# Kernel optimization log

Hardware: AMD Instinct MI355X
Metric: run time of the kernel (lower is better)

Reference implementation:

```python
import jax, jax.numpy as jnp
import numpy as np

C, K, H = 256, 64, 1024


def squash(t):
    # t: [C, H]; norm = sum of squares over last dim (matches torch code)
    norm = jnp.sum(t * t, axis=-1, keepdims=True)  # [C, 1]
    scale = norm / (1.0 + norm)
    return scale * t / jnp.sqrt(norm)


def setup_inputs() -> dict:
    key = jax.random.key(0)
    k1, k2 = jax.random.split(key)
    encoder_output = jax.random.normal(k1, (C, K, H), dtype=jnp.float32)
    # nn.Linear weight [out, in]; scaled init for numerical sanity
    W = jax.random.normal(k2, (H, H), dtype=jnp.float32) * (1.0 / np.sqrt(H))
    return {"encoder_output": encoder_output, "W": W, "iter_routing": 3}


def reference(encoder_output, W, iter_routing):
    # encoder_output: [C, K, H], W: [H, H] (l_1 weight, no bias)
    # The linear projection is loop-invariant in the original; hoist it.
    x_hat = jnp.einsum('ckh,dh->ckd', encoder_output, W)  # [C, K, H]
    b = jnp.zeros(encoder_output.shape[:2], dtype=encoder_output.dtype)  # [C, K]
    c = None
    for _ in range(iter_routing):
        d = jax.nn.softmax(b, axis=-1)                       # [C, K]
        c_hat = jnp.sum(x_hat * d[..., None], axis=1)        # [C, H]
        c = squash(c_hat)                                    # [C, H]
        b = b + jnp.einsum('ckh,ch->ck', x_hat, c)           # [C, K]
    return c
```

## Files before the change

### kernel.cpp

```cpp
#include <hip/hip_runtime.h>


using f32x4  = __attribute__((ext_vector_type(4))) float;
using f32x2  = __attribute__((ext_vector_type(2))) float;
using bf16x8 = __attribute__((ext_vector_type(8))) __bf16;
using bf16x2 = __attribute__((ext_vector_type(2))) __bf16;

struct BfPair { __bf16 hi, lo; };
__device__ inline BfPair split_bf16(float x) {
    BfPair p;
    p.hi = (__bf16)x;
    p.lo = (__bf16)(x - (float)p.hi);
    return p;
}

template <int MODE>
__global__ __launch_bounds__(1024) void routing_kernel(
    const float* __restrict__ enc, const float* __restrict__ u0,
    const float* __restrict__ u1, float* __restrict__ bglob,
    __bf16* __restrict__ s_hi, __bf16* __restrict__ s_lo)
{
    __shared__ float spart[16][1024];
    __shared__ float b_s[64];
    __shared__ float d_s[64];

    const int t = threadIdx.x, lane = t & 63, w = t >> 6;
    const int c = blockIdx.x;
    const float* E = enc + (size_t)c * 65536;

    f32x4 er[4][4];
    #pragma unroll
    for (int r = 0; r < 4; ++r) {
        const float* ek = E + (size_t)(w * 4 + r) * 1024 + lane * 8;
        er[r][0] = *(const f32x4*)(ek);
        er[r][1] = *(const f32x4*)(ek + 4);
        er[r][2] = *(const f32x4*)(ek + 512);
        er[r][3] = *(const f32x4*)(ek + 516);
    }

    if (MODE > 0) {
        const size_t ub = (size_t)c * 1024 + lane * 8;
        f32x4 uf[4];
        #pragma unroll
        for (int q = 0; q < 4; ++q) {
            const size_t o = ub + (q >> 1) * 512 + (q & 1) * 4;
            uf[q] = *(const f32x4*)(u0 + o) + *(const f32x4*)(u1 + o);
        }
        #pragma unroll
        for (int r = 0; r < 4; ++r) {
            float sum = 0.f;
            #pragma unroll
            for (int q = 0; q < 4; ++q)
                #pragma unroll
                for (int j = 0; j < 4; ++j)
                    sum += er[r][q][j] * uf[q][j];
            #pragma unroll
            for (int off = 32; off; off >>= 1) sum += __shfl_xor(sum, off, 64);
            if (lane == 0) {
                const int k = w * 4 + r;
                const float bv = (MODE == 2) ? (bglob[c * 64 + k] + sum) : sum;
                bglob[c * 64 + k] = bv;
                b_s[k] = bv;
            }
        }
    }
    __syncthreads();

    if (MODE == 0) {
        if (t < 64) d_s[t] = 1.f / 64.f;
    } else if (t < 64) {
        float bv = b_s[t], m = bv;
        #pragma unroll
        for (int off = 32; off; off >>= 1) m = fmaxf(m, __shfl_xor(m, off, 64));
        const float e = expf(bv - m);
        float sm = e;
        #pragma unroll
        for (int off = 32; off; off >>= 1) sm += __shfl_xor(sm, off, 64);
        d_s[t] = e / sm;
    }
    __syncthreads();

    #pragma unroll
    for (int q = 0; q < 4; ++q) {
        f32x4 p = {};
        #pragma unroll
        for (int r = 0; r < 4; ++r) {
            const float dk = d_s[w * 4 + r];
            #pragma unroll
            for (int j = 0; j < 4; ++j) p[j] += dk * er[r][q][j];
        }
        const int h = (q >> 1) * 512 + lane * 8 + (q & 1) * 4;
        *(f32x4*)&spart[w][h] = p;
    }
    __syncthreads();

    {
        float a = 0.f;
        #pragma unroll
        for (int wv = 0; wv < 16; ++wv) a += spart[wv][t];
        const BfPair p = split_bf16(a);
        s_hi[(size_t)c * 1024 + t] = p.hi;
        s_lo[(size_t)c * 1024 + t] = p.lo;
    }
}

__global__ __launch_bounds__(256) void gemm_split_kernel(
    const __bf16* __restrict__ Ah, const __bf16* __restrict__ Al,
    const __bf16* __restrict__ Bh, const __bf16* __restrict__ Bl,
    float* __restrict__ C0, float* __restrict__ C1)
{
    const int w = threadIdx.x >> 6;
    const int gw = blockIdx.x * 4 + w;
    const int task = gw >> 1;
    const int kh   = gw & 1;
    const int mt   = task >> 6;
    const int nt   = task & 63;
    const int lane = threadIdx.x & 63;
    const int kq   = (lane >> 4) * 8 + kh * 512;
    const size_t aoff = (size_t)(mt * 16 + (lane & 15)) * 1024 + kq;
    const size_t boff = (size_t)(nt * 16 + (lane & 15)) * 1024 + kq;

    f32x4 hh = {}, hl = {}, lh = {};
    #pragma unroll 4
    for (int k0 = 0; k0 < 512; k0 += 32) {
        bf16x8 ah = *(const bf16x8*)(Ah + aoff + k0);
        bf16x8 al = *(const bf16x8*)(Al + aoff + k0);
        bf16x8 bh = *(const bf16x8*)(Bh + boff + k0);
        bf16x8 bl = *(const bf16x8*)(Bl + boff + k0);
        hh = __builtin_amdgcn_mfma_f32_16x16x32_bf16(ah, bh, hh, 0, 0, 0);
        hl = __builtin_amdgcn_mfma_f32_16x16x32_bf16(ah, bl, hl, 0, 0, 0);
        lh = __builtin_amdgcn_mfma_f32_16x16x32_bf16(al, bh, lh, 0, 0, 0);
    }
    f32x4 acc = hh + hl + lh;
    float* Cc = kh ? C1 : C0;
    const int rr = (lane >> 4) * 4, colb = lane & 15;
    #pragma unroll
    for (int r = 0; r < 4; ++r)
        Cc[(size_t)(mt * 16 + rr + r) * 1024 + nt * 16 + colb] = acc[r];
}

__global__ __launch_bounds__(256) void squash_kernel(
    const float* __restrict__ chat0, const float* __restrict__ chat1,
    __bf16* __restrict__ c_hi, __bf16* __restrict__ c_lo,
    float* __restrict__ outp)
{
    __shared__ float wsum[4];
    const int c = blockIdx.x, t = threadIdx.x;
    const int lane = t & 63, w = t >> 6;
    const int h0 = t * 4;
    const size_t o = (size_t)c * 1024 + h0;
    f32x4 v = *(const f32x4*)(chat0 + o) + *(const f32x4*)(chat1 + o);
    float ss = v[0]*v[0] + v[1]*v[1] + v[2]*v[2] + v[3]*v[3];
    #pragma unroll
    for (int off = 32; off; off >>= 1) ss += __shfl_xor(ss, off, 64);
    if (lane == 0) wsum[w] = ss;
    __syncthreads();
    const float norm = wsum[0] + wsum[1] + wsum[2] + wsum[3];
    const float scale = norm / ((1.f + norm) * sqrtf(norm) + 1e-30f);
    f32x4 ov;
    __attribute__((ext_vector_type(4))) __bf16 hv, lv;
    #pragma unroll
    for (int j = 0; j < 4; ++j) {
        ov[j] = v[j] * scale;
        const BfPair p = split_bf16(ov[j]);
        hv[j] = p.hi; lv[j] = p.lo;
    }
    *(f32x4*)(outp + o) = ov;
    *(__attribute__((ext_vector_type(4))) __bf16*)(c_hi + o) = hv;
    *(__attribute__((ext_vector_type(4))) __bf16*)(c_lo + o) = lv;
}

__global__ __launch_bounds__(256) void convert_w_kernel(
    const float* __restrict__ W, __bf16* __restrict__ Wb_hi,
    __bf16* __restrict__ Wb_lo, __bf16* __restrict__ Wt_hi,
    __bf16* __restrict__ Wt_lo)
{
    __shared__ float tile[64][65];
    const int bx = blockIdx.x, by = blockIdx.y;
    const int tx = threadIdx.x & 63, ty = threadIdx.x >> 6;
    for (int i = ty; i < 64; i += 4) {
        const size_t idx = (size_t)(by * 64 + i) * 1024 + bx * 64 + tx;
        const float v = W[idx];
        tile[i][tx] = v;
        const BfPair p = split_bf16(v);
        Wb_hi[idx] = p.hi; Wb_lo[idx] = p.lo;
    }
    __syncthreads();
    for (int i = ty; i < 64; i += 4) {
        const size_t idx = (size_t)(bx * 64 + i) * 1024 + by * 64 + tx;
        const BfPair p = split_bf16(tile[tx][i]);
        Wt_hi[idx] = p.hi; Wt_lo[idx] = p.lo;
    }
}

__global__ __launch_bounds__(512) void fallback_kernel(
    const float* __restrict__ enc, const float* __restrict__ W,
    float* __restrict__ outp)
{
    __shared__ float u_s[1024], s_s[1024], c_s[1024], chat_s[1024];
    __shared__ float b_s[64], d_s[64], red_s[8];
    const int t = threadIdx.x, lane = t & 63, w = t >> 6;
    const float* erow = enc + (size_t)blockIdx.x * 65536;

    if (t < 64) b_s[t] = 0.f;
    __syncthreads();

    for (int it = 0; it < 3; ++it) {
        if (it > 0) {
            f32x4 uf[4];
            #pragma unroll
            for (int q = 0; q < 2; ++q) {
                uf[2*q]   = *(const f32x4*)&u_s[q*512 + lane*8];
                uf[2*q+1] = *(const f32x4*)&u_s[q*512 + lane*8 + 4];
            }
            for (int r = 0; r < 8; ++r) {
                const int k = w * 8 + r;
                const float* ek = erow + (size_t)k * 1024;
                float sum = 0.f;
                #pragma unroll
                for (int q = 0; q < 2; ++q) {
                    f32x4 e0 = *(const f32x4*)(ek + q*512 + lane*8);
                    f32x4 e1 = *(const f32x4*)(ek + q*512 + lane*8 + 4);
                    #pragma unroll
                    for (int j = 0; j < 4; ++j) {
                        sum += e0[j] * uf[2*q][j];
                        sum += e1[j] * uf[2*q+1][j];
                    }
                }
                #pragma unroll
                for (int off = 32; off; off >>= 1) sum += __shfl_xor(sum, off, 64);
                if (lane == 0) b_s[k] += sum;
            }
            __syncthreads();
        }
        if (t < 64) {
            float bv = b_s[t], m = bv;
            #pragma unroll
            for (int off = 32; off; off >>= 1) m = fmaxf(m, __shfl_xor(m, off, 64));
            float e = expf(bv - m), sm = e;
            #pragma unroll
            for (int off = 32; off; off >>= 1) sm += __shfl_xor(sm, off, 64);
            d_s[t] = e / sm;
        }
        __syncthreads();
        {
            const int h0 = t * 2;
            float a0 = 0.f, a1 = 0.f;
            for (int k = 0; k < 64; ++k) {
                f32x2 ev = *(const f32x2*)(erow + (size_t)k * 1024 + h0);
                a0 += d_s[k] * ev[0]; a1 += d_s[k] * ev[1];
            }
            s_s[h0] = a0; s_s[h0+1] = a1;
        }
        __syncthreads();
        {
            f32x4 sf[4];
            #pragma unroll
            for (int q = 0; q < 2; ++q) {
                sf[2*q]   = *(const f32x4*)&s_s[q*512 + lane*8];
                sf[2*q+1] = *(const f32x4*)&s_s[q*512 + lane*8 + 4];
            }
            for (int r = 0; r < 128; ++r) {
                const int d = w * 128 + r;
                const float* wr = W + (size_t)d * 1024;
                float sum = 0.f;
                #pragma unroll
                for (int q = 0; q < 2; ++q) {
                    f32x4 w0 = *(const f32x4*)(wr + q*512 + lane*8);
                    f32x4 w1 = *(const f32x4*)(wr + q*512 + lane*8 + 4);
                    #pragma unroll
                    for (int j = 0; j < 4; ++j) {
                        sum += w0[j] * sf[2*q][j];
                        sum += w1[j] * sf[2*q+1][j];
                    }
                }
                #pragma unroll
                for (int off = 32; off; off >>= 1) sum += __shfl_xor(sum, off, 64);
                if (lane == 0) chat_s[d] = sum;
            }
        }
        __syncthreads();
        {
            const int h0 = t * 2;
            float v0 = chat_s[h0], v1 = chat_s[h0+1];
            float ss = v0*v0 + v1*v1;
            #pragma unroll
            for (int off = 32; off; off >>= 1) ss += __shfl_xor(ss, off, 64);
            if (lane == 0) red_s[w] = ss;
            __syncthreads();
            float norm = 0.f;
            #pragma unroll
            for (int i = 0; i < 8; ++i) norm += red_s[i];
            const float scale = norm / ((1.f + norm) * sqrtf(norm) + 1e-30f);
            c_s[h0] = v0 * scale; c_s[h0+1] = v1 * scale;
        }
        __syncthreads();
        if (it < 2) {
            const int h0 = t * 2;
            float uu0 = 0.f, uu1 = 0.f;
            for (int d = 0; d < 1024; ++d) {
                f32x2 wv = *(const f32x2*)(W + (size_t)d * 1024 + h0);
                uu0 += c_s[d] * wv[0]; uu1 += c_s[d] * wv[1];
            }
            u_s[h0] = uu0; u_s[h0+1] = uu1;
        } else {
            const int h0 = t * 2;
            f32x2 ov; ov[0] = c_s[h0]; ov[1] = c_s[h0+1];
            *(f32x2*)(outp + (size_t)blockIdx.x * 1024 + h0) = ov;
        }
        __syncthreads();
    }
}

extern "C" void kernel_launch(void* const* d_in, const int* in_sizes, int n_in,
                              void* d_out, int out_size, void* d_ws, size_t ws_size,
                              hipStream_t stream)
{
    const float* enc = (const float*)d_in[0];
    const float* W   = (const float*)d_in[1];
    float* outp = (float*)d_out;
    (void)in_sizes; (void)n_in; (void)out_size;

    char* ws = (char*)d_ws;
    float*  b     = (float*) (ws + 0x000000);
    __bf16* s_hi  = (__bf16*)(ws + 0x080000);
    __bf16* s_lo  = (__bf16*)(ws + 0x100000);
    __bf16* c_hi  = (__bf16*)(ws + 0x180000);
    __bf16* c_lo  = (__bf16*)(ws + 0x200000);
    float*  chat0 = (float*) (ws + 0x280000);
    float*  chat1 = (float*) (ws + 0x380000);
    float*  u0    = (float*) (ws + 0x480000);
    float*  u1    = (float*) (ws + 0x580000);
    __bf16* Wb_hi = (__bf16*)(ws + 0x680000);
    __bf16* Wb_lo = (__bf16*)(ws + 0x880000);
    __bf16* Wt_hi = (__bf16*)(ws + 0xA80000);
    __bf16* Wt_lo = (__bf16*)(ws + 0xC80000);

    if (ws_size < 0xE80000) {
        fallback_kernel<<<256, 512, 0, stream>>>(enc, W, outp);
        return;
    }

    convert_w_kernel<<<dim3(16, 16), 256, 0, stream>>>(W, Wb_hi, Wb_lo,
                                                       Wt_hi, Wt_lo);

    routing_kernel<0><<<256, 1024, 0, stream>>>(enc, u0, u1, b, s_hi, s_lo);
    gemm_split_kernel<<<512, 256, 0, stream>>>(s_hi, s_lo, Wb_hi, Wb_lo,
                                               chat0, chat1);
    squash_kernel<<<256, 256, 0, stream>>>(chat0, chat1, c_hi, c_lo, outp);
    gemm_split_kernel<<<512, 256, 0, stream>>>(c_hi, c_lo, Wt_hi, Wt_lo,
                                               u0, u1);
    routing_kernel<1><<<256, 1024, 0, stream>>>(enc, u0, u1, b, s_hi, s_lo);
    gemm_split_kernel<<<512, 256, 0, stream>>>(s_hi, s_lo, Wb_hi, Wb_lo,
                                               chat0, chat1);
    squash_kernel<<<256, 256, 0, stream>>>(chat0, chat1, c_hi, c_lo, outp);
    gemm_split_kernel<<<512, 256, 0, stream>>>(c_hi, c_lo, Wt_hi, Wt_lo,
                                               u0, u1);
    routing_kernel<2><<<256, 1024, 0, stream>>>(enc, u0, u1, b, s_hi, s_lo);
    gemm_split_kernel<<<512, 256, 0, stream>>>(s_hi, s_lo, Wb_hi, Wb_lo,
                                               chat0, chat1);
    squash_kernel<<<256, 256, 0, stream>>>(chat0, chat1, c_hi, c_lo, outp);
}
```

Before: 216.6 us.

## Precompute W^T W Gram matrix to merge projection GEMMs and fuse squash into routing

Uses the identity that the agreement term x_hat·c equals enc·(W^T W s)·scale. The code computes Q = W^T W once, in extra blocks of the first routing launch, so each routing iteration needs only one GEMM (s·Q) instead of two. The squash scale is recomputed inside the routing kernel from s·(Qs), which removes the intermediate squash kernels. The W conversion is folded into spare blocks of the first GEMM launch. This cuts kernel launches and GEMM work, but adds a 1024^3 Gram GEMM and changes the rounding path through a split-bf16 Q.

```diff
diff --git a/kernel.cpp b/kernel.cpp
--- a/kernel.cpp
+++ b/kernel.cpp
@@ -4,7 +4,7 @@
 using f32x4  = __attribute__((ext_vector_type(4))) float;
 using f32x2  = __attribute__((ext_vector_type(2))) float;
 using bf16x8 = __attribute__((ext_vector_type(8))) __bf16;
-using bf16x2 = __attribute__((ext_vector_type(2))) __bf16;
+using bf16x4 = __attribute__((ext_vector_type(4))) __bf16;
 
 struct BfPair { __bf16 hi, lo; };
 __device__ inline BfPair split_bf16(float x) {
@@ -15,18 +15,23 @@
 }
 
 template <int MODE>
-__global__ __launch_bounds__(1024) void routing_kernel(
-    const float* __restrict__ enc, const float* __restrict__ u0,
-    const float* __restrict__ u1, float* __restrict__ bglob,
-    __bf16* __restrict__ s_hi, __bf16* __restrict__ s_lo)
-{
-    __shared__ float spart[16][1024];
-    __shared__ float b_s[64];
-    __shared__ float d_s[64];
-
+__device__ __forceinline__ void routing_body(
+    const float* __restrict__ enc, const float* __restrict__ y0,
+    const float* __restrict__ y1, float* __restrict__ bglob,
+    __bf16* __restrict__ s_hi, __bf16* __restrict__ s_lo,
+    float (*spart)[1024], float* u_s, float* b_s, float* d_s,
+    float* red_s, float* scale_s)
+{
     const int t = threadIdx.x, lane = t & 63, w = t >> 6;
     const int c = blockIdx.x;
     const float* E = enc + (size_t)c * 65536;
+
+    float yv = 0.f, sv = 0.f;
+    if (MODE > 0) {
+        const size_t o = (size_t)c * 1024 + t;
+        yv = y0[o] + y1[o];
+        sv = (float)s_hi[o] + (float)s_lo[o];
+    }
 
     f32x4 er[4][4];
     #pragma unroll
@@ -39,13 +44,25 @@
     }
 
     if (MODE > 0) {
-        const size_t ub = (size_t)c * 1024 + lane * 8;
+        u_s[t] = yv;
+        float p = yv * sv;
+        #pragma unroll
+        for (int off = 32; off; off >>= 1) p += __shfl_xor(p, off, 64);
+        if (lane == 0) red_s[w] = p;
+        __syncthreads();
+        if (t == 0) {
+            float n = 0.f;
+            #pragma unroll
+            for (int i = 0; i < 16; ++i) n += red_s[i];
+            *scale_s = n / ((1.f + n) * sqrtf(n) + 1e-30f);
+        }
+        __syncthreads();
+        const float scale = *scale_s;
         f32x4 uf[4];
-        #pragma unroll
-        for (int q = 0; q < 4; ++q) {
-            const size_t o = ub + (q >> 1) * 512 + (q & 1) * 4;
-            uf[q] = *(const f32x4*)(u0 + o) + *(const f32x4*)(u1 + o);
-        }
+        uf[0] = *(const f32x4*)&u_s[lane * 8];
+        uf[1] = *(const f32x4*)&u_s[lane * 8 + 4];
+        uf[2] = *(const f32x4*)&u_s[512 + lane * 8];
+        uf[3] = *(const f32x4*)&u_s[512 + lane * 8 + 4];
         #pragma unroll
         for (int r = 0; r < 4; ++r) {
             float sum = 0.f;
@@ -58,7 +75,8 @@
             for (int off = 32; off; off >>= 1) sum += __shfl_xor(sum, off, 64);
             if (lane == 0) {
                 const int k = w * 4 + r;
-                const float bv = (MODE == 2) ? (bglob[c * 64 + k] + sum) : sum;
+                const float bv =
+                    (MODE == 2 ? bglob[c * 64 + k] : 0.f) + scale * sum;
                 bglob[c * 64 + k] = bv;
                 b_s[k] = bv;
             }
@@ -104,11 +122,106 @@
     }
 }
 
+__device__ __forceinline__ void gemm_q_body(
+    const __bf16* __restrict__ Wt_hi, const __bf16* __restrict__ Wt_lo,
+    __bf16* __restrict__ Q_hi, __bf16* __restrict__ Q_lo, int task, int lane)
+{
+    const int i = task >> 5, j = task & 31;
+    const int kq = (lane >> 4) * 8;
+    const size_t a0 = (size_t)(i * 32 + (lane & 15)) * 1024 + kq;
+    const size_t a1 = a0 + 16 * 1024;
+    const size_t b0 = (size_t)(j * 32 + (lane & 15)) * 1024 + kq;
+    const size_t b1 = b0 + 16 * 1024;
+
+    f32x4 acc[2][2] = {};
+    #pragma unroll 2
+    for (int k0 = 0; k0 < 1024; k0 += 32) {
+        bf16x8 ah[2], al[2], bh[2], bl[2];
+        ah[0] = *(const bf16x8*)(Wt_hi + a0 + k0);
+        ah[1] = *(const bf16x8*)(Wt_hi + a1 + k0);
+        al[0] = *(const bf16x8*)(Wt_lo + a0 + k0);
+        al[1] = *(const bf16x8*)(Wt_lo + a1 + k0);
+        bh[0] = *(const bf16x8*)(Wt_hi + b0 + k0);
+        bh[1] = *(const bf16x8*)(Wt_hi + b1 + k0);
+        bl[0] = *(const bf16x8*)(Wt_lo + b0 + k0);
+        bl[1] = *(const bf16x8*)(Wt_lo + b1 + k0);
+        #pragma unroll
+        for (int mi = 0; mi < 2; ++mi)
+            #pragma unroll
+            for (int ni = 0; ni < 2; ++ni) {
+                f32x4 a = acc[mi][ni];
+                a = __builtin_amdgcn_mfma_f32_16x16x32_bf16(ah[mi], bh[ni], a, 0, 0, 0);
+                a = __builtin_amdgcn_mfma_f32_16x16x32_bf16(ah[mi], bl[ni], a, 0, 0, 0);
+                a = __builtin_amdgcn_mfma_f32_16x16x32_bf16(al[mi], bh[ni], a, 0, 0, 0);
+                acc[mi][ni] = a;
+            }
+    }
+    const int rr = (lane >> 4) * 4, colb = lane & 15;
+    #pragma unroll
+    for (int mi = 0; mi < 2; ++mi)
+        #pragma unroll
+        for (int ni = 0; ni < 2; ++ni)
+            #pragma unroll
+            for (int r = 0; r < 4; ++r) {
+                const BfPair p = split_bf16(acc[mi][ni][r]);
+                const size_t idx =
+                    (size_t)(i * 32 + mi * 16 + rr + r) * 1024 +
+                    j * 32 + ni * 16 + colb;
+                Q_hi[idx] = p.hi;
+                Q_lo[idx] = p.lo;
+            }
+}
+
+template <int MODE, int WITH_Q>
+__global__ __launch_bounds__(1024) void routing_q_kernel(
+    const float* __restrict__ enc, const float* __restrict__ y0,
+    const float* __restrict__ y1, float* __restrict__ bglob,
+    __bf16* __restrict__ s_hi, __bf16* __restrict__ s_lo,
+    const __bf16* __restrict__ Wt_hi, const __bf16* __restrict__ Wt_lo,
+    __bf16* __restrict__ Q_hi, __bf16* __restrict__ Q_lo)
+{
+    __shared__ float spart[16][1024];
+    __shared__ float u_s[1024];
+    __shared__ float b_s[64], d_s[64], red_s[16], scale_s;
+
+    if (WITH_Q && blockIdx.x >= 256) {
+        const int w = threadIdx.x >> 6, lane = threadIdx.x & 63;
+        gemm_q_body(Wt_hi, Wt_lo, Q_hi, Q_lo,
+                    (blockIdx.x - 256) * 16 + w, lane);
+        return;
+    }
+    routing_body<MODE>(enc, y0, y1, bglob, s_hi, s_lo,
+                       spart, u_s, b_s, d_s, red_s, &scale_s);
+}
+
+template <int CONV>
 __global__ __launch_bounds__(256) void gemm_split_kernel(
     const __bf16* __restrict__ Ah, const __bf16* __restrict__ Al,
     const __bf16* __restrict__ Bh, const __bf16* __restrict__ Bl,
-    float* __restrict__ C0, float* __restrict__ C1)
-{
+    float* __restrict__ C0, float* __restrict__ C1,
+    const float* __restrict__ Wsrc, __bf16* __restrict__ Wd_hi,
+    __bf16* __restrict__ Wd_lo)
+{
+    if (CONV && blockIdx.x >= 512) {
+        const int b = blockIdx.x - 512;
+        const size_t base = (size_t)b * 4096 + (threadIdx.x << 2);
+        #pragma unroll
+        for (int q = 0; q < 4; ++q) {
+            const size_t idx = base + (size_t)q * 1024;
+            const f32x4 v = *(const f32x4*)(Wsrc + idx);
+            bf16x4 hv, lv;
+            #pragma unroll
+            for (int j = 0; j < 4; ++j) {
+                const BfPair p = split_bf16(v[j]);
+                hv[j] = p.hi;
+                lv[j] = p.lo;
+            }
+            *(bf16x4*)(Wd_hi + idx) = hv;
+            *(bf16x4*)(Wd_lo + idx) = lv;
+        }
+        return;
+    }
+
     const int w = threadIdx.x >> 6;
     const int gw = blockIdx.x * 4 + w;
     const int task = gw >> 1;
@@ -139,16 +252,14 @@
         Cc[(size_t)(mt * 16 + rr + r) * 1024 + nt * 16 + colb] = acc[r];
 }
 
-__global__ __launch_bounds__(256) void squash_kernel(
+__global__ __launch_bounds__(256) void squash_out_kernel(
     const float* __restrict__ chat0, const float* __restrict__ chat1,
-    __bf16* __restrict__ c_hi, __bf16* __restrict__ c_lo,
     float* __restrict__ outp)
 {
     __shared__ float wsum[4];
     const int c = blockIdx.x, t = threadIdx.x;
     const int lane = t & 63, w = t >> 6;
-    const int h0 = t * 4;
-    const size_t o = (size_t)c * 1024 + h0;
+    const size_t o = (size_t)c * 1024 + t * 4;
     f32x4 v = *(const f32x4*)(chat0 + o) + *(const f32x4*)(chat1 + o);
     float ss = v[0]*v[0] + v[1]*v[1] + v[2]*v[2] + v[3]*v[3];
     #pragma unroll
@@ -157,39 +268,24 @@
     __syncthreads();
     const float norm = wsum[0] + wsum[1] + wsum[2] + wsum[3];
     const float scale = norm / ((1.f + norm) * sqrtf(norm) + 1e-30f);
-    f32x4 ov;
-    __attribute__((ext_vector_type(4))) __bf16 hv, lv;
-    #pragma unroll
-    for (int j = 0; j < 4; ++j) {
-        ov[j] = v[j] * scale;
-        const BfPair p = split_bf16(ov[j]);
-        hv[j] = p.hi; lv[j] = p.lo;
-    }
-    *(f32x4*)(outp + o) = ov;
-    *(__attribute__((ext_vector_type(4))) __bf16*)(c_hi + o) = hv;
-    *(__attribute__((ext_vector_type(4))) __bf16*)(c_lo + o) = lv;
-}
-
-__global__ __launch_bounds__(256) void convert_w_kernel(
-    const float* __restrict__ W, __bf16* __restrict__ Wb_hi,
-    __bf16* __restrict__ Wb_lo, __bf16* __restrict__ Wt_hi,
+    *(f32x4*)(outp + o) = v * scale;
+}
+
+__global__ __launch_bounds__(256) void convert_wt_kernel(
+    const float* __restrict__ W, __bf16* __restrict__ Wt_hi,
     __bf16* __restrict__ Wt_lo)
 {
     __shared__ float tile[64][65];
     const int bx = blockIdx.x, by = blockIdx.y;
     const int tx = threadIdx.x & 63, ty = threadIdx.x >> 6;
-    for (int i = ty; i < 64; i += 4) {
-        const size_t idx = (size_t)(by * 64 + i) * 1024 + bx * 64 + tx;
-        const float v = W[idx];
-        tile[i][tx] = v;
-        const BfPair p = split_bf16(v);
-        Wb_hi[idx] = p.hi; Wb_lo[idx] = p.lo;
-    }
+    for (int i = ty; i < 64; i += 4)
+        tile[i][tx] = W[(size_t)(by * 64 + i) * 1024 + bx * 64 + tx];
     __syncthreads();
     for (int i = ty; i < 64; i += 4) {
         const size_t idx = (size_t)(bx * 64 + i) * 1024 + by * 64 + tx;
         const BfPair p = split_bf16(tile[tx][i]);
-        Wt_hi[idx] = p.hi; Wt_lo[idx] = p.lo;
+        Wt_hi[idx] = p.hi;
+        Wt_lo[idx] = p.lo;
     }
 }
 
@@ -325,39 +421,37 @@
     float*  b     = (float*) (ws + 0x000000);
     __bf16* s_hi  = (__bf16*)(ws + 0x080000);
     __bf16* s_lo  = (__bf16*)(ws + 0x100000);
-    __bf16* c_hi  = (__bf16*)(ws + 0x180000);
-    __bf16* c_lo  = (__bf16*)(ws + 0x200000);
-    float*  chat0 = (float*) (ws + 0x280000);
-    float*  chat1 = (float*) (ws + 0x380000);
-    float*  u0    = (float*) (ws + 0x480000);
-    float*  u1    = (float*) (ws + 0x580000);
-    __bf16* Wb_hi = (__bf16*)(ws + 0x680000);
-    __bf16* Wb_lo = (__bf16*)(ws + 0x880000);
-    __bf16* Wt_hi = (__bf16*)(ws + 0xA80000);
-    __bf16* Wt_lo = (__bf16*)(ws + 0xC80000);
-
-    if (ws_size < 0xE80000) {
+    float*  y0    = (float*) (ws + 0x180000);
+    float*  y1    = (float*) (ws + 0x280000);
+    __bf16* Wx_hi = (__bf16*)(ws + 0x380000);
+    __bf16* Wx_lo = (__bf16*)(ws + 0x580000);
+    __bf16* Q_hi  = (__bf16*)(ws + 0x780000);
+    __bf16* Q_lo  = (__bf16*)(ws + 0x980000);
+
+    if (ws_size < 0xB80000) {
         fallback_kernel<<<256, 512, 0, stream>>>(enc, W, outp);
         return;
     }
 
-    convert_w_kernel<<<dim3(16, 16), 256, 0, stream>>>(W, Wb_hi, Wb_lo,
-                                                       Wt_hi, Wt_lo);
-
-    routing_kernel<0><<<256, 1024, 0, stream>>>(enc, u0, u1, b, s_hi, s_lo);
-    gemm_split_kernel<<<512, 256, 0, stream>>>(s_hi, s_lo, Wb_hi, Wb_lo,
-                                               chat0, chat1);
-    squash_kernel<<<256, 256, 0, stream>>>(chat0, chat1, c_hi, c_lo, outp);
-    gemm_split_kernel<<<512, 256, 0, stream>>>(c_hi, c_lo, Wt_hi, Wt_lo,
-                                               u0, u1);
-    routing_kernel<1><<<256, 1024, 0, stream>>>(enc, u0, u1, b, s_hi, s_lo);
-    gemm_split_kernel<<<512, 256, 0, stream>>>(s_hi, s_lo, Wb_hi, Wb_lo,
-                                               chat0, chat1);
-    squash_kernel<<<256, 256, 0, stream>>>(chat0, chat1, c_hi, c_lo, outp);
-    gemm_split_kernel<<<512, 256, 0, stream>>>(c_hi, c_lo, Wt_hi, Wt_lo,
-                                               u0, u1);
-    routing_kernel<2><<<256, 1024, 0, stream>>>(enc, u0, u1, b, s_hi, s_lo);
-    gemm_split_kernel<<<512, 256, 0, stream>>>(s_hi, s_lo, Wb_hi, Wb_lo,
-                                               chat0, chat1);
-    squash_kernel<<<256, 256, 0, stream>>>(chat0, chat1, c_hi, c_lo, outp);
-}
+    convert_wt_kernel<<<dim3(16, 16), 256, 0, stream>>>(W, Wx_hi, Wx_lo);
+
+    routing_q_kernel<0, 1><<<320, 1024, 0, stream>>>(
+        enc, y0, y1, b, s_hi, s_lo, Wx_hi, Wx_lo, Q_hi, Q_lo);
+
+    gemm_split_kernel<1><<<768, 256, 0, stream>>>(
+        s_hi, s_lo, Q_hi, Q_lo, y0, y1, W, Wx_hi, Wx_lo);
+
+    routing_q_kernel<1, 0><<<256, 1024, 0, stream>>>(
+        enc, y0, y1, b, s_hi, s_lo, Wx_hi, Wx_lo, Q_hi, Q_lo);
+
+    gemm_split_kernel<0><<<512, 256, 0, stream>>>(
+        s_hi, s_lo, Q_hi, Q_lo, y0, y1, nullptr, nullptr, nullptr);
+
+    routing_q_kernel<2, 0><<<256, 1024, 0, stream>>>(
+        enc, y0, y1, b, s_hi, s_lo, Wx_hi, Wx_lo, Q_hi, Q_lo);
+
+    gemm_split_kernel<0><<<512, 256, 0, stream>>>(
+        s_hi, s_lo, Wx_hi, Wx_lo, y0, y1, nullptr, nullptr, nullptr);
+
+    squash_out_kernel<<<256, 256, 0, stream>>>(y0, y1, outp);
+}
```

Result: slower. 289.9 us (+33.8%).
